# Kernel tuning notes

Measured on AMD Instinct MI355X. Metric: run time of the kernel, lower is better.

Reference implementation:

```python
import jax, jax.numpy as jnp
import numpy as np

B, T, F, D, H, HD = 1, 16, 256, 768, 12, 64
NUM_LOOKBACK = 6  # remaining H - NUM_LOOKBACK heads are lookahead


def setup_inputs() -> dict:
    key = jax.random.key(0)
    ks = jax.random.split(key, 9)
    s = 0.02
    return {
        "x": jax.random.normal(ks[0], (B, T, F, D), dtype=jnp.float32),
        "Wq": jax.random.normal(ks[1], (H, D, HD), dtype=jnp.float32) * s,
        "bq": jax.random.normal(ks[2], (H, HD), dtype=jnp.float32) * s,
        "Wk": jax.random.normal(ks[3], (H, D, HD), dtype=jnp.float32) * s,
        "bk": jax.random.normal(ks[4], (H, HD), dtype=jnp.float32) * s,
        "Wv": jax.random.normal(ks[5], (H, D, HD), dtype=jnp.float32) * s,
        "bv": jax.random.normal(ks[6], (H, HD), dtype=jnp.float32) * s,
        "Wo": jax.random.normal(ks[7], (D, D), dtype=jnp.float32) * s,
        "bo": jax.random.normal(ks[8], (D,), dtype=jnp.float32) * s,
    }


def reference(x, Wq, bq, Wk, bk, Wv, bv, Wo, bo):
    b, t, f, d = x.shape
    tf = t * f
    xf = x.reshape(b, tf, d)

    # batched per-head projections: [b, h, n, hd]
    q = jnp.einsum('bnd,hdk->bhnk', xf, Wq) + bq[None, :, None, :]
    k = jnp.einsum('bnd,hdk->bhnk', xf, Wk) + bk[None, :, None, :]
    v = jnp.einsum('bnd,hdk->bhnk', xf, Wv) + bv[None, :, None, :]

    scale = 1.0 / jnp.sqrt(jnp.asarray(q.shape[-1], dtype=q.dtype))
    scores = jnp.einsum('bhqd,bhkd->bhqk', q, k) * scale  # [b,h,tf,tf]

    # lookback mask == causal (q_idx >= kv_idx); lookahead == anti-causal
    idx = jnp.arange(tf)
    causal = idx[:, None] >= idx[None, :]
    neg = jnp.finfo(scores.dtype).min
    s_lb = jnp.where(causal[None, None], scores[:, :NUM_LOOKBACK], neg)
    s_la = jnp.where(causal.T[None, None], scores[:, NUM_LOOKBACK:], neg)
    scores = jnp.concatenate([s_lb, s_la], axis=1)

    p = jax.nn.softmax(scores, axis=-1)
    o = jnp.einsum('bhqk,bhkd->bhqd', p, v)  # [b,h,tf,hd]
    o = o.transpose(0, 2, 1, 3).reshape(b, tf, d)  # concat heads on feature dim

    out = o @ Wo + bo
    return out.reshape(b, t, f, d)
```

## Files before the change

### kernel.cpp

```cpp
#include <hip/hip_runtime.h>
#include <hip/hip_bf16.h>

typedef __attribute__((ext_vector_type(4))) float f32x4;
typedef __attribute__((ext_vector_type(8))) short s16x8;
typedef __attribute__((ext_vector_type(4))) int i32x4;
typedef __attribute__((address_space(3))) unsigned char lds_t;
typedef __attribute__((address_space(1))) const unsigned char glob_t;

#define TFDIM 4096
#define DMODEL 768
#define NHEAD 12
#define HDIM 64
#define NLB 6

static __device__ __forceinline__ unsigned short f2bf(float f) {
    union { float f; unsigned u; } x; x.f = f;
    unsigned r = x.u + 0x7fff + ((x.u >> 16) & 1);
    return (unsigned short)(r >> 16);
}

static __device__ __forceinline__ float exp2_hw(float x) {
    float r;
    asm("v_exp_f32 %0, %1\n\ts_nop 0" : "=v"(r) : "v"(x));
    return r;
}

static __device__ __forceinline__ unsigned cvtpk_bf16(float lo, float hi) {
    unsigned r;
    asm("v_cvt_pk_bf16_f32 %0, %1, %2" : "=v"(r) : "v"(lo), "v"(hi));
    return r;
}

static __device__ __forceinline__ void xpose_pair(unsigned& a, unsigned& b) {
    asm volatile("v_permlane32_swap_b32 %0, %1" : "+v"(a), "+v"(b));
    asm volatile("v_permlane16_swap_b32 %0, %1" : "+v"(a), "+v"(b));
}

__global__ __launch_bounds__(256) void prep_kernel(
    const float* __restrict__ x, unsigned short* __restrict__ xb,
    const float* __restrict__ Wq, const float* __restrict__ Wk, const float* __restrict__ Wv,
    const float* __restrict__ bq, const float* __restrict__ bk, const float* __restrict__ bv,
    unsigned short* __restrict__ Wt, float* __restrict__ bias,
    const float* __restrict__ Wo, unsigned short* __restrict__ Wot,
    float* __restrict__ Lacc) {
    __shared__ unsigned short tile[64][65];
    int b = blockIdx.x;
    int t = threadIdx.x;
    if (b < 432) {
        int qkv = b / 144, rem = b - qkv * 144, h = rem / 12, kt = rem - h * 12;
        const float* W = (qkv == 0) ? Wq : ((qkv == 1) ? Wk : Wv);
        int trow = t >> 2, tco = (t & 3) << 4;
        const float* src = &W[((size_t)h * 768 + kt * 64 + trow) * 64 + tco];
#pragma unroll
        for (int j = 0; j < 4; j++) {
            float4 v = *(const float4*)&src[j * 4];
            tile[trow][tco + j * 4 + 0] = f2bf(v.x);
            tile[trow][tco + j * 4 + 1] = f2bf(v.y);
            tile[trow][tco + j * 4 + 2] = f2bf(v.z);
            tile[trow][tco + j * 4 + 3] = f2bf(v.w);
        }
        if (kt == 0 && t < 64) {
            const float* bb = (qkv == 0) ? bq : ((qkv == 1) ? bk : bv);
            bias[qkv * 768 + h * 64 + t] = bb[h * 64 + t];
        }
        __syncthreads();
        unsigned short vals[16];
#pragma unroll
        for (int j = 0; j < 16; j++) vals[j] = tile[tco + j][trow];
        unsigned short* dst = &Wt[(size_t)(qkv * 768 + h * 64 + trow) * 768 + kt * 64 + tco];
        *(s16x8*)&dst[0] = *(const s16x8*)&vals[0];
        *(s16x8*)&dst[8] = *(const s16x8*)&vals[8];
    } else if (b < 576) {
        int bb = b - 432;
        int nt = bb / 12, kt = bb - nt * 12;
        int trow = t >> 2, tco = (t & 3) << 4;
        const float* src = &Wo[(size_t)(kt * 64 + trow) * 768 + nt * 64 + tco];
#pragma unroll
        for (int j = 0; j < 4; j++) {
            float4 v = *(const float4*)&src[j * 4];
            tile[trow][tco + j * 4 + 0] = f2bf(v.x);
            tile[trow][tco + j * 4 + 1] = f2bf(v.y);
            tile[trow][tco + j * 4 + 2] = f2bf(v.z);
            tile[trow][tco + j * 4 + 3] = f2bf(v.w);
        }
        __syncthreads();
        unsigned short vals[16];
#pragma unroll
        for (int j = 0; j < 16; j++) vals[j] = tile[tco + j][trow];
        unsigned short* dst = &Wot[(size_t)(nt * 64 + trow) * 768 + kt * 64 + tco];
        *(s16x8*)&dst[0] = *(const s16x8*)&vals[0];
        *(s16x8*)&dst[8] = *(const s16x8*)&vals[8];
    } else if (b < 624) {
        int i = (b - 576) * 256 + t;
        if (i < NHEAD * TFDIM / 4) {
            float4 z = {0.f, 0.f, 0.f, 0.f};
            ((float4*)Lacc)[i] = z;
        }
    } else {
        int i = (b - 624) * 256 + t;
        if (i < TFDIM * DMODEL / 4) {
            float4 v = ((const float4*)x)[i];
            ushort4 o;
            o.x = f2bf(v.x); o.y = f2bf(v.y); o.z = f2bf(v.z); o.w = f2bf(v.w);
            ((ushort4*)xb)[i] = o;
        }
    }
}

template <int EPI, int ANORM>
__global__ __launch_bounds__(256) void gemm_bt_kernel(
    const unsigned short* __restrict__ A,
    const float* __restrict__ Af32, const float* __restrict__ Lacc,
    const unsigned short* __restrict__ Bt,
    const float* __restrict__ bias,
    float* __restrict__ Cf, unsigned short* __restrict__ Cb,
    unsigned short* __restrict__ Vtg,
    int M, int N, int K) {
    __shared__ __align__(16) unsigned short As[128 * 64];
    __shared__ __align__(16) unsigned short Bs[128 * 64];
    int tid = threadIdx.x;
    int w = tid >> 6, l = tid & 63, lr = l & 15, lg = l >> 4;
    int wm = w >> 1, wn = w & 1;

    int nwg = gridDim.x * gridDim.y;
    int flat = blockIdx.y * gridDim.x + blockIdx.x;
    int cpx = nwg >> 3;
    int swz = (flat & 7) * cpx + (flat >> 3);
    int bx = swz % gridDim.x, by = swz / gridDim.x;
    size_t mbase = (size_t)by * 128, nbase = (size_t)bx * 128;

    int drw = l >> 3, dslot = l & 7;
    int dg = (dslot ^ drw) << 3;
    f32x4 acc[4][4] = {};
    for (int k0 = 0; k0 < K; k0 += 64) {
        __syncthreads();
        if (ANORM) {
#pragma unroll
            for (int i = 0; i < 4; i++) {
                int idx = tid + i * 256;
                int row = idx >> 3, g = idx & 7;
                const float* src = &Af32[(mbase + row) * K + k0 + g * 8];
                float4 a0 = *(const float4*)&src[0];
                float4 a1 = *(const float4*)&src[4];
                float rl = __builtin_amdgcn_rcpf(Lacc[(size_t)(k0 >> 6) * TFDIM + mbase + row]);
                unsigned short us[8];
                us[0] = f2bf(a0.x * rl); us[1] = f2bf(a0.y * rl);
                us[2] = f2bf(a0.z * rl); us[3] = f2bf(a0.w * rl);
                us[4] = f2bf(a1.x * rl); us[5] = f2bf(a1.y * rl);
                us[6] = f2bf(a1.z * rl); us[7] = f2bf(a1.w * rl);
                *(s16x8*)&As[row * 64 + ((g ^ (row & 7)) << 3)] = *(const s16x8*)us;
            }
        } else {
#pragma unroll
            for (int j = 0; j < 4; j++) {
                int row = j * 32 + w * 8 + drw;
                __builtin_amdgcn_global_load_lds((glob_t*)&A[(mbase + row) * K + k0 + dg],
                                                 (lds_t*)&As[(j * 32 + w * 8) * 64], 16, 0, 0);
            }
        }
#pragma unroll
        for (int j = 0; j < 4; j++) {
            int row = j * 32 + w * 8 + drw;
            __builtin_amdgcn_global_load_lds((glob_t*)&Bt[(nbase + row) * K + k0 + dg],
                                             (lds_t*)&Bs[(j * 32 + w * 8) * 64], 16, 0, 0);
        }
        __syncthreads();
#pragma unroll
        for (int ks = 0; ks < 2; ks++) {
            s16x8 af[4], bfr[4];
#pragma unroll
            for (int m = 0; m < 4; m++) {
                int row = wm * 64 + m * 16 + lr;
                af[m] = *(const s16x8*)&As[row * 64 + (((ks * 4 + lg) ^ (row & 7)) << 3)];
            }
#pragma unroll
            for (int n = 0; n < 4; n++) {
                int row = wn * 64 + n * 16 + lr;
                bfr[n] = *(const s16x8*)&Bs[row * 64 + (((ks * 4 + lg) ^ (row & 7)) << 3)];
            }
#pragma unroll
            for (int m = 0; m < 4; m++)
#pragma unroll
                for (int n = 0; n < 4; n++)
                    acc[m][n] = __builtin_amdgcn_mfma_f32_16x16x32_bf16(af[m], bfr[n], acc[m][n], 0, 0, 0);
        }
    }
#pragma unroll
    for (int m = 0; m < 4; m++) {
        size_t row0 = mbase + wm * 64 + m * 16 + lg * 4;
#pragma unroll
        for (int n = 0; n < 4; n++) {
            size_t col = nbase + wn * 64 + n * 16 + lr;
            float bv = bias[col];
#pragma unroll
            for (int r = 0; r < 4; r++) {
                float v = acc[m][n][r] + bv;
                if (EPI == 0) {
                    Cf[(row0 + r) * N + col] = v;
                } else if (col < 1536) {
                    if (col < 768) v *= 0.18033688f;
                    Cb[(((col >> 6) * 4096 + (row0 + r)) << 6) + (col & 63)] = f2bf(v);
                } else {
                    Vtg[(size_t)(((col - 1536) >> 6) * 262144) + (col & 63) * 4096 + (row0 + r)] = f2bf(v);
                }
            }
        }
    }
}

__global__ __launch_bounds__(512, 4) void attn_kernel(const unsigned short* __restrict__ qk,
                                                      const unsigned short* __restrict__ vtg,
                                                      float* __restrict__ Oacc,
                                                      float* __restrict__ Lacc) {
    __shared__ __align__(16) unsigned short Ks[3][64][64];
    __shared__ __align__(16) unsigned short Vs[3][64][64];

    int b = blockIdx.x;
    int h = b % NHEAD;
    int idx = 79 - (b / NHEAD);
    int jqw, c, n;
    if (idx < 8)       { jqw = idx;               c = 0;              n = 1; }
    else if (idx < 24) { jqw = 8 + ((idx - 8) >> 1);  c = (idx - 8) & 1;  n = 2; }
    else if (idx < 48) { jqw = 16 + (idx - 24) / 3;   c = (idx - 24) % 3; n = 3; }
    else               { jqw = 24 + ((idx - 48) >> 2); c = (idx - 48) & 3; n = 4; }
    int W = 2 * jqw + 2;
    int base = W / n, rem = W % n;
    int len = base + (c < rem ? 1 : 0);
    int s0 = c * base + (c < rem ? c : rem);
    bool causal = (h < NLB);
    int jq = causal ? jqw : (31 - jqw);
    int qbase = jq * 128;
    int dkb = 2 * jq;
    int kb0 = (causal ? 0 : (62 - 2 * jqw)) + s0;
    int kb1 = kb0 + len - 1;

    const unsigned short* Q  = qk + (size_t)h * TFDIM * HDIM;
    const unsigned short* Kp = qk + (size_t)(NHEAD + h) * TFDIM * HDIM;
    const unsigned short* Vt = vtg + (size_t)h * HDIM * TFDIM;

    int tid = threadIdx.x, w = tid >> 6, l = tid & 63, lr = l & 15, lg = l >> 4;
    int qh = w >> 2, wq = w & 3;
    int dk = dkb + qh;

    s16x8 qf[2];
    {
        size_t qrow = (size_t)(qbase + qh * 64 + wq * 16 + lr);
        qf[0] = *(const s16x8*)&Q[qrow * HDIM + lg * 8];
        qf[1] = *(const s16x8*)&Q[qrow * HDIM + 32 + lg * 8];
    }
    f32x4 oacc[4] = {};
    float lsum = 0.f;

    int drow = tid >> 3, dseg = tid & 7;
    int sg0 = (dseg ^ (drow & 7)) << 3;
    auto stage = [&](int buf, int kv) {
        __builtin_amdgcn_global_load_lds((glob_t*)(Kp + (size_t)(kv * 64 + drow) * HDIM + sg0),
                                         (lds_t*)&Ks[buf][w * 8][0], 16, 0, 0);
        __builtin_amdgcn_global_load_lds((glob_t*)(Vt + (size_t)drow * TFDIM + kv * 64 + sg0),
                                         (lds_t*)&Vs[buf][w * 8][0], 16, 0, 0);
    };

    stage(0, kb0);

    int cur = 0;
    int qcol = wq * 16 + lr;
    for (int kb = kb0; kb <= kb1; kb++) {
        bool more = (kb < kb1);
        if (more) {
            int nxt = (cur == 2) ? 0 : cur + 1;
            stage(nxt, kb + 1);
            asm volatile("s_waitcnt vmcnt(2)" ::: "memory");
        } else {
            asm volatile("s_waitcnt vmcnt(0)" ::: "memory");
        }
        __builtin_amdgcn_s_barrier();
        __builtin_amdgcn_sched_barrier(0);

        int kvbase = kb * 64;
        s16x8 vf[2][4];
#pragma unroll
        for (int ks = 0; ks < 2; ks++)
#pragma unroll
            for (int df = 0; df < 4; df++)
                vf[ks][df] = *(const s16x8*)&Vs[cur][df * 16 + lr][(ks * 32 + lg * 8) ^ ((lr & 7) << 3)];
        f32x4 s[4];
        __builtin_amdgcn_s_setprio(1);
#pragma unroll
        for (int f = 0; f < 4; f++) {
            s16x8 kf0 = *(const s16x8*)&Ks[cur][f * 16 + lr][(lg * 8) ^ ((lr & 7) << 3)];
            s16x8 kf1 = *(const s16x8*)&Ks[cur][f * 16 + lr][(32 + lg * 8) ^ ((lr & 7) << 3)];
            f32x4 z = {0.f, 0.f, 0.f, 0.f};
            z = __builtin_amdgcn_mfma_f32_16x16x32_bf16(kf0, qf[0], z, 0, 0, 0);
            z = __builtin_amdgcn_mfma_f32_16x16x32_bf16(kf1, qf[1], z, 0, 0, 0);
            s[f] = z;
        }
        __builtin_amdgcn_s_setprio(0);

        bool skip = causal ? (kb > dk) : (kb < dk);
        if (!skip) {
            if (kb == dk) {
                int qi = qbase + qh * 64 + qcol;
#pragma unroll
                for (int f = 0; f < 4; f++)
#pragma unroll
                    for (int r = 0; r < 4; r++) {
                        int ki = kvbase + f * 16 + lg * 4 + r;
                        bool keep = causal ? (qi >= ki) : (qi <= ki);
                        if (!keep) s[f][r] = -1e30f;
                    }
            }
            float ls = 0.f;
            unsigned w0[4], w1[4];
#pragma unroll
            for (int f = 0; f < 4; f++) {
                float p0 = exp2_hw(s[f][0]);
                float p1 = exp2_hw(s[f][1]);
                float p2 = exp2_hw(s[f][2]);
                float p3 = exp2_hw(s[f][3]);
                ls += (p0 + p1) + (p2 + p3);
                w0[f] = cvtpk_bf16(p0, p1);
                w1[f] = cvtpk_bf16(p2, p3);
            }
            lsum += ls;
            xpose_pair(w0[0], w0[1]);
            xpose_pair(w1[0], w1[1]);
            xpose_pair(w0[2], w0[3]);
            xpose_pair(w1[2], w1[3]);
            union { unsigned u[4]; s16x8 v8; } pk0, pk1;
            pk0.u[0] = w0[0]; pk0.u[1] = w1[0]; pk0.u[2] = w0[1]; pk0.u[3] = w1[1];
            pk1.u[0] = w0[2]; pk1.u[1] = w1[2]; pk1.u[2] = w0[3]; pk1.u[3] = w1[3];
            __builtin_amdgcn_s_setprio(1);
#pragma unroll
            for (int df = 0; df < 4; df++) {
                oacc[df] = __builtin_amdgcn_mfma_f32_16x16x32_bf16(pk0.v8, vf[0][df], oacc[df], 0, 0, 0);
                oacc[df] = __builtin_amdgcn_mfma_f32_16x16x32_bf16(pk1.v8, vf[1][df], oacc[df], 0, 0, 0);
            }
            __builtin_amdgcn_s_setprio(0);
        }

        cur = (cur == 2) ? 0 : cur + 1;
    }
    lsum += __shfl_xor(lsum, 16);
    lsum += __shfl_xor(lsum, 32);
    if (lg == 0)
        atomicAdd(&Lacc[h * TFDIM + qbase + qh * 64 + wq * 16 + lr], lsum);
#pragma unroll
    for (int df = 0; df < 4; df++)
#pragma unroll
        for (int r = 0; r < 4; r++) {
            int row = qbase + qh * 64 + wq * 16 + lg * 4 + r;
            atomicAdd(&Oacc[(size_t)row * DMODEL + h * HDIM + df * 16 + lr], oacc[df][r]);
        }
}

__global__ void merge_kernel(const float* __restrict__ Oacc, const float* __restrict__ Lacc,
                             unsigned short* __restrict__ ob) {
    int i = blockIdx.x * 256 + threadIdx.x;
    if (i >= TFDIM * DMODEL / 4) return;
    int col4 = i % (DMODEL / 4), row = i / (DMODEL / 4);
    float4 v = ((const float4*)Oacc)[i];
    int h = col4 >> 4;
    float rl = 1.0f / Lacc[h * TFDIM + row];
    ushort4 u;
    u.x = f2bf(v.x * rl); u.y = f2bf(v.y * rl); u.z = f2bf(v.z * rl); u.w = f2bf(v.w * rl);
    ((ushort4*)ob)[i] = u;
}


extern "C" void kernel_launch(void* const* d_in, const int* in_sizes, int n_in,
                              void* d_out, int out_size, void* d_ws, size_t ws_size,
                              hipStream_t stream) {
    const float* x  = (const float*)d_in[0];
    const float* Wq = (const float*)d_in[1];
    const float* bq = (const float*)d_in[2];
    const float* Wk = (const float*)d_in[3];
    const float* bk = (const float*)d_in[4];
    const float* Wv = (const float*)d_in[5];
    const float* bv = (const float*)d_in[6];
    const float* Wo = (const float*)d_in[7];
    const float* bo = (const float*)d_in[8];
    float* out = (float*)d_out;
    char* ws = (char*)d_ws;
    const unsigned short* dummyA = (const unsigned short*)d_ws;

    if (ws_size >= 32833536) {
        float*          Oacc = (float*)(ws + 0);
        unsigned short* xb   = (unsigned short*)(ws + 0);
        unsigned short* WtQ  = (unsigned short*)(ws + 6291456);
        float*          bqkv = (float*)(ws + 9830400);
        unsigned short* qkb  = (unsigned short*)(ws + 12582912);
        unsigned short* vtg  = (unsigned short*)(ws + 25165824);
        unsigned short* Wot  = (unsigned short*)(ws + 31457280);
        float*          Lacc = (float*)(ws + 32636928);

        prep_kernel<<<3696, 256, 0, stream>>>(x, xb, Wq, Wk, Wv, bq, bk, bv, WtQ, bqkv, Wo, Wot, Lacc);

        dim3 g1(2304 / 128, 4096 / 128);
        gemm_bt_kernel<1, 0><<<g1, 256, 0, stream>>>(xb, nullptr, nullptr, WtQ, bqkv, nullptr, qkb, vtg, 4096, 2304, 768);

        hipMemsetAsync(Oacc, 0, (size_t)TFDIM * DMODEL * 4, stream);

        attn_kernel<<<960, 512, 0, stream>>>(qkb, vtg, Oacc, Lacc);

        dim3 g3(768 / 128, 4096 / 128);
        gemm_bt_kernel<0, 1><<<g3, 256, 0, stream>>>(dummyA, Oacc, Lacc, Wot, bo, out, nullptr, nullptr, 4096, 768, 768);
    } else {
        unsigned short* xb   = (unsigned short*)(ws + 0);
        unsigned short* ob   = (unsigned short*)(ws + 0);
        unsigned short* WtQ  = (unsigned short*)(ws + 6291456);
        unsigned short* Wot  = (unsigned short*)(ws + 9830400);
        float*          bqkv = (float*)(ws + 11010048);
        unsigned short* qkb  = (unsigned short*)(ws + 11019264);
        unsigned short* vtg  = (unsigned short*)(ws + 23602176);
        float*          Lacc = (float*)(ws + 29893632);
        float*          Oacc = out;

        hipMemsetAsync(Oacc, 0, (size_t)TFDIM * DMODEL * 4, stream);
        prep_kernel<<<3696, 256, 0, stream>>>(x, xb, Wq, Wk, Wv, bq, bk, bv, WtQ, bqkv, Wo, Wot, Lacc);

        dim3 g1(2304 / 128, 4096 / 128);
        gemm_bt_kernel<1, 0><<<g1, 256, 0, stream>>>(xb, nullptr, nullptr, WtQ, bqkv, nullptr, qkb, vtg, 4096, 2304, 768);

        attn_kernel<<<960, 512, 0, stream>>>(qkb, vtg, Oacc, Lacc);
        merge_kernel<<<(TFDIM * DMODEL / 4 + 255) / 256, 256, 0, stream>>>(Oacc, Lacc, ob);

        dim3 g3(768 / 128, 4096 / 128);
        gemm_bt_kernel<0, 0><<<g3, 256, 0, stream>>>(ob, nullptr, nullptr, Wot, bo, out, nullptr, nullptr, 4096, 768, 768);
    }
}
```

Before: 128.2 us.

## Fuse x bf16 conversion into QKV GEMM, remap attention blocks, deepen prefetch

```diff
diff --git a/kernel.cpp b/kernel.cpp
--- a/kernel.cpp
+++ b/kernel.cpp
@@ -37,7 +37,6 @@
 }
 
 __global__ __launch_bounds__(256) void prep_kernel(
-    const float* __restrict__ x, unsigned short* __restrict__ xb,
     const float* __restrict__ Wq, const float* __restrict__ Wk, const float* __restrict__ Wv,
     const float* __restrict__ bq, const float* __restrict__ bk, const float* __restrict__ bv,
     unsigned short* __restrict__ Wt, float* __restrict__ bias,
@@ -90,24 +89,16 @@
         unsigned short* dst = &Wot[(size_t)(nt * 64 + trow) * 768 + kt * 64 + tco];
         *(s16x8*)&dst[0] = *(const s16x8*)&vals[0];
         *(s16x8*)&dst[8] = *(const s16x8*)&vals[8];
-    } else if (b < 624) {
+    } else {
         int i = (b - 576) * 256 + t;
         if (i < NHEAD * TFDIM / 4) {
             float4 z = {0.f, 0.f, 0.f, 0.f};
             ((float4*)Lacc)[i] = z;
         }
-    } else {
-        int i = (b - 624) * 256 + t;
-        if (i < TFDIM * DMODEL / 4) {
-            float4 v = ((const float4*)x)[i];
-            ushort4 o;
-            o.x = f2bf(v.x); o.y = f2bf(v.y); o.z = f2bf(v.z); o.w = f2bf(v.w);
-            ((ushort4*)xb)[i] = o;
-        }
-    }
-}
-
-template <int EPI, int ANORM>
+    }
+}
+
+template <int EPI, int AX>
 __global__ __launch_bounds__(256) void gemm_bt_kernel(
     const unsigned short* __restrict__ A,
     const float* __restrict__ Af32, const float* __restrict__ Lacc,
@@ -134,7 +125,7 @@
     f32x4 acc[4][4] = {};
     for (int k0 = 0; k0 < K; k0 += 64) {
         __syncthreads();
-        if (ANORM) {
+        if (AX >= 1) {
 #pragma unroll
             for (int i = 0; i < 4; i++) {
                 int idx = tid + i * 256;
@@ -142,12 +133,19 @@
                 const float* src = &Af32[(mbase + row) * K + k0 + g * 8];
                 float4 a0 = *(const float4*)&src[0];
                 float4 a1 = *(const float4*)&src[4];
-                float rl = __builtin_amdgcn_rcpf(Lacc[(size_t)(k0 >> 6) * TFDIM + mbase + row]);
                 unsigned short us[8];
-                us[0] = f2bf(a0.x * rl); us[1] = f2bf(a0.y * rl);
-                us[2] = f2bf(a0.z * rl); us[3] = f2bf(a0.w * rl);
-                us[4] = f2bf(a1.x * rl); us[5] = f2bf(a1.y * rl);
-                us[6] = f2bf(a1.z * rl); us[7] = f2bf(a1.w * rl);
+                if (AX == 2) {
+                    float rl = __builtin_amdgcn_rcpf(Lacc[(size_t)(k0 >> 6) * TFDIM + mbase + row]);
+                    us[0] = f2bf(a0.x * rl); us[1] = f2bf(a0.y * rl);
+                    us[2] = f2bf(a0.z * rl); us[3] = f2bf(a0.w * rl);
+                    us[4] = f2bf(a1.x * rl); us[5] = f2bf(a1.y * rl);
+                    us[6] = f2bf(a1.z * rl); us[7] = f2bf(a1.w * rl);
+                } else {
+                    us[0] = f2bf(a0.x); us[1] = f2bf(a0.y);
+                    us[2] = f2bf(a0.z); us[3] = f2bf(a0.w);
+                    us[4] = f2bf(a1.x); us[5] = f2bf(a1.y);
+                    us[6] = f2bf(a1.z); us[7] = f2bf(a1.w);
+                }
                 *(s16x8*)&As[row * 64 + ((g ^ (row & 7)) << 3)] = *(const s16x8*)us;
             }
         } else {
@@ -216,8 +214,21 @@
     __shared__ __align__(16) unsigned short Vs[3][64][64];
 
     int b = blockIdx.x;
-    int h = b % NHEAD;
-    int idx = 79 - (b / NHEAD);
+    int xc = b & 7, j = b >> 3;
+    int t3 = j / 3, rsel = j - t3 * 3;
+    int h, r;
+    if (xc & 1) {
+        int ffull = (3 * xc + 1) >> 1;
+        if (rsel == 0)      { h = ffull;     r = 2 * t3; }
+        else if (rsel == 1) { h = ffull;     r = 2 * t3 + 1; }
+        else                { h = ffull - 1; r = 2 * t3 + 1; }
+    } else {
+        int ffull = (3 * xc) >> 1;
+        if (rsel == 0)      { h = ffull;     r = 2 * t3; }
+        else if (rsel == 1) { h = ffull;     r = 2 * t3 + 1; }
+        else                { h = ffull + 1; r = 2 * t3; }
+    }
+    int idx = 79 - r;
     int jqw, c, n;
     if (idx < 8)       { jqw = idx;               c = 0;              n = 1; }
     else if (idx < 24) { jqw = 8 + ((idx - 8) >> 1);  c = (idx - 8) & 1;  n = 2; }
@@ -261,20 +272,23 @@
     };
 
     stage(0, kb0);
+    if (kb0 + 1 <= kb1) stage(1, kb0 + 1);
 
     int cur = 0;
     int qcol = wq * 16 + lr;
     for (int kb = kb0; kb <= kb1; kb++) {
         bool more = (kb < kb1);
         if (more) {
-            int nxt = (cur == 2) ? 0 : cur + 1;
-            stage(nxt, kb + 1);
             asm volatile("s_waitcnt vmcnt(2)" ::: "memory");
         } else {
             asm volatile("s_waitcnt vmcnt(0)" ::: "memory");
         }
         __builtin_amdgcn_s_barrier();
         __builtin_amdgcn_sched_barrier(0);
+        if (kb + 2 <= kb1) {
+            int n2 = cur + 2; if (n2 >= 3) n2 -= 3;
+            stage(n2, kb + 2);
+        }
 
         int kvbase = kb * 64;
         s16x8 vf[2][4];
@@ -303,10 +317,10 @@
 #pragma unroll
                 for (int f = 0; f < 4; f++)
 #pragma unroll
-                    for (int r = 0; r < 4; r++) {
-                        int ki = kvbase + f * 16 + lg * 4 + r;
+                    for (int r2 = 0; r2 < 4; r2++) {
+                        int ki = kvbase + f * 16 + lg * 4 + r2;
                         bool keep = causal ? (qi >= ki) : (qi <= ki);
-                        if (!keep) s[f][r] = -1e30f;
+                        if (!keep) s[f][r2] = -1e30f;
                     }
             }
             float ls = 0.f;
@@ -347,9 +361,9 @@
 #pragma unroll
     for (int df = 0; df < 4; df++)
 #pragma unroll
-        for (int r = 0; r < 4; r++) {
-            int row = qbase + qh * 64 + wq * 16 + lg * 4 + r;
-            atomicAdd(&Oacc[(size_t)row * DMODEL + h * HDIM + df * 16 + lr], oacc[df][r]);
+        for (int r2 = 0; r2 < 4; r2++) {
+            int row = qbase + qh * 64 + wq * 16 + lg * 4 + r2;
+            atomicAdd(&Oacc[(size_t)row * DMODEL + h * HDIM + df * 16 + lr], oacc[df][r2]);
         }
 }
 
@@ -385,7 +399,6 @@
 
     if (ws_size >= 32833536) {
         float*          Oacc = (float*)(ws + 0);
-        unsigned short* xb   = (unsigned short*)(ws + 0);
         unsigned short* WtQ  = (unsigned short*)(ws + 6291456);
         float*          bqkv = (float*)(ws + 9830400);
         unsigned short* qkb  = (unsigned short*)(ws + 12582912);
@@ -393,19 +406,18 @@
         unsigned short* Wot  = (unsigned short*)(ws + 31457280);
         float*          Lacc = (float*)(ws + 32636928);
 
-        prep_kernel<<<3696, 256, 0, stream>>>(x, xb, Wq, Wk, Wv, bq, bk, bv, WtQ, bqkv, Wo, Wot, Lacc);
+        prep_kernel<<<624, 256, 0, stream>>>(Wq, Wk, Wv, bq, bk, bv, WtQ, bqkv, Wo, Wot, Lacc);
 
         dim3 g1(2304 / 128, 4096 / 128);
-        gemm_bt_kernel<1, 0><<<g1, 256, 0, stream>>>(xb, nullptr, nullptr, WtQ, bqkv, nullptr, qkb, vtg, 4096, 2304, 768);
+        gemm_bt_kernel<1, 1><<<g1, 256, 0, stream>>>(dummyA, x, nullptr, WtQ, bqkv, nullptr, qkb, vtg, 4096, 2304, 768);
 
         hipMemsetAsync(Oacc, 0, (size_t)TFDIM * DMODEL * 4, stream);
 
         attn_kernel<<<960, 512, 0, stream>>>(qkb, vtg, Oacc, Lacc);
 
         dim3 g3(768 / 128, 4096 / 128);
-        gemm_bt_kernel<0, 1><<<g3, 256, 0, stream>>>(dummyA, Oacc, Lacc, Wot, bo, out, nullptr, nullptr, 4096, 768, 768);
+        gemm_bt_kernel<0, 2><<<g3, 256, 0, stream>>>(dummyA, Oacc, Lacc, Wot, bo, out, nullptr, nullptr, 4096, 768, 768);
     } else {
-        unsigned short* xb   = (unsigned short*)(ws + 0);
         unsigned short* ob   = (unsigned short*)(ws + 0);
         unsigned short* WtQ  = (unsigned short*)(ws + 6291456);
         unsigned short* Wot  = (unsigned short*)(ws + 9830400);
@@ -416,10 +428,10 @@
         float*          Oacc = out;
 
         hipMemsetAsync(Oacc, 0, (size_t)TFDIM * DMODEL * 4, stream);
-        prep_kernel<<<3696, 256, 0, stream>>>(x, xb, Wq, Wk, Wv, bq, bk, bv, WtQ, bqkv, Wo, Wot, Lacc);
+        prep_kernel<<<624, 256, 0, stream>>>(Wq, Wk, Wv, bq, bk, bv, WtQ, bqkv, Wo, Wot, Lacc);
 
         dim3 g1(2304 / 128, 4096 / 128);
-        gemm_bt_kernel<1, 0><<<g1, 256, 0, stream>>>(xb, nullptr, nullptr, WtQ, bqkv, nullptr, qkb, vtg, 4096, 2304, 768);
+        gemm_bt_kernel<1, 1><<<g1, 256, 0, stream>>>(dummyA, x, nullptr, WtQ, bqkv, nullptr, qkb, vtg, 4096, 2304, 768);
 
         attn_kernel<<<960, 512, 0, stream>>>(qkb, vtg, Oacc, Lacc);
         merge_kernel<<<(TFDIM * DMODEL / 4 + 255) / 256, 256, 0, stream>>>(Oacc, Lacc, ob);
```

Result: slower. 146.1 us (+14.0%).
